# Performance work log

Measured on AMD Instinct MI355X. Metric: run time of the kernel, lower is better.

Reference implementation:

```python
import jax, jax.numpy as jnp
import numpy as np

WS = 8        # window size (square)
TW = 8        # total windows per side = input_resolution // WS
NH = 16       # num heads


def make_indices(ws, tw):
    # local relative position index (N, N)
    c = np.stack(np.meshgrid(np.arange(ws), np.arange(ws), indexing='ij')).reshape(2, -1)
    rel = (c[:, :, None] - c[:, None, :]).transpose(1, 2, 0).astype(np.int64)
    rel[..., 0] += ws - 1
    rel[..., 1] += ws - 1
    rel[..., 0] *= 2 * ws - 1
    local_idx = rel.sum(-1)
    # global (window-token -> window-grid) relative position index (N, tw*tw)
    ck = np.stack(np.meshgrid(np.arange(tw), np.arange(tw), indexing='ij')).reshape(2, -1)
    relg = (c[:, :, None] - ck[:, None, :]).transpose(1, 2, 0).astype(np.int64)
    relg[..., 0] += tw - 1
    relg[..., 1] += tw - 1
    relg[..., 0] *= ws + tw - 1
    global_idx = relg.sum(-1)
    return local_idx, global_idx


def setup_inputs() -> dict:
    key = jax.random.key(0)
    ks = jax.random.split(key, 13)
    B, H, W, C = 16, 64, 64, 512
    s = 0.02
    return {
        'x': jax.random.normal(ks[0], (B, H, W, C), jnp.float32),
        'qkv_w': jax.random.normal(ks[1], (C, 3 * C), jnp.float32) * s,
        'qkv_b': jax.random.normal(ks[2], (3 * C,), jnp.float32) * s,
        'local_bias_table': jax.random.normal(ks[3], ((2 * WS - 1) ** 2, NH), jnp.float32) * s,
        'global_bias_table': jax.random.normal(ks[4], ((WS + TW - 1) ** 2, NH), jnp.float32) * s,
        'local_proj_w': jax.random.normal(ks[5], (C, C), jnp.float32) * s,
        'local_proj_b': jax.random.normal(ks[6], (C,), jnp.float32) * s,
        'pool_w': jnp.full((WS * WS,), 1.0 / (WS * WS) * (WS * WS), jnp.float32) * 0 + jax.random.normal(ks[7], (WS * WS,), jnp.float32) * s + 1.0 / (WS * WS),
        'pool_b': jnp.zeros((1,), jnp.float32),
        'global_proj_w': jax.random.normal(ks[8], (C, C), jnp.float32) * s,
        'global_proj_b': jax.random.normal(ks[9], (C,), jnp.float32) * s,
        'pfc_w': jax.random.normal(ks[10], (2 * C, C), jnp.float32) * s,
        'pfc_b': jax.random.normal(ks[11], (C,), jnp.float32) * s,
    }


def reference(x, qkv_w, qkv_b, local_bias_table, global_bias_table,
              local_proj_w, local_proj_b, pool_w, pool_b,
              global_proj_w, global_proj_b, pfc_w, pfc_b):
    B, H, W, C = x.shape
    N = WS * WS                      # tokens per window
    nWs = (H // WS) * (W // WS)      # number of windows
    B_ = B * nWs
    hd = C // NH
    scale = hd ** -0.5

    local_idx, global_idx = make_indices(WS, H // WS)

    # NOTE: faithful to original — qkv applied to x in row-major order,
    # then reshaped into (B_, N, ...) chunks (window_partition output is unused).
    qkv = (x.reshape(-1, C) @ qkv_w + qkv_b).reshape(B_, N, 3, NH, hd)
    qkv = qkv.transpose(2, 0, 3, 1, 4)  # (3, B_, NH, N, hd)
    q, k, v = qkv[0], qkv[1], qkv[2]

    # ---- fine (local window) attention ----
    lb = local_bias_table[local_idx.reshape(-1)].reshape(N, N, NH).transpose(2, 0, 1)
    fine = jax.nn.softmax(jnp.einsum('bhnd,bhmd->bhnm', q * scale, k) + lb[None])
    fine_out = jnp.einsum('bhnm,bhmd->bnhd', fine, v).reshape(B_, N, C)
    fine_out = fine_out @ local_proj_w + local_proj_b

    # ---- coarse (pooled global) attention ----
    k5 = k.reshape(B, nWs, NH, N, hd)
    v5 = v.reshape(B, nWs, NH, N, hd)
    # pooled over the N window-token axis; original uses pool_layer_k for BOTH K and V
    Kg = jnp.einsum('bwhnd,n->bhwd', k5, pool_w) + pool_b  # (B, NH, nWs, hd)
    Vg = jnp.einsum('bwhnd,n->bhwd', v5, pool_w) + pool_b
    Kb = jnp.broadcast_to(Kg[:, None], (B, nWs, NH, nWs, hd)).reshape(B_, NH, nWs, hd)
    Vb = jnp.broadcast_to(Vg[:, None], (B, nWs, NH, nWs, hd)).reshape(B_, NH, nWs, hd)

    gb = global_bias_table[global_idx.reshape(-1)].reshape(N, nWs, NH).transpose(2, 0, 1)
    coarse = jax.nn.softmax(jnp.einsum('bhnd,bhwd->bhnw', q * scale, Kb) + gb[None])
    coarse_out = jnp.einsum('bhnw,bhwd->bnhd', coarse, Vb).reshape(B_, N, C)
    coarse_out = coarse_out @ global_proj_w + global_proj_b

    # ---- fused projection ----
    out = jnp.concatenate([fine_out, coarse_out], axis=-1) @ pfc_w + pfc_b
    return out  # (B_, N, C)
```

## Files before the change

kernel.cpp:

```cpp
#include <hip/hip_runtime.h>


typedef unsigned int u32;
typedef _Float16 f16;
typedef __attribute__((ext_vector_type(8))) _Float16 f16x8;
typedef __attribute__((ext_vector_type(4))) float f32x4;
typedef __attribute__((ext_vector_type(4))) u32 u32x4;

__device__ __forceinline__ f32x4 mfma_16x16x32(f16x8 a, f16x8 b, f32x4 c) {
  return __builtin_amdgcn_mfma_f32_16x16x32_f16(a, b, c, 0, 0, 0);
}

__device__ __forceinline__ void async_cp16(const void* g, void* l) {
  __builtin_amdgcn_global_load_lds(
      (const __attribute__((address_space(1))) u32*)g,
      (__attribute__((address_space(3))) u32*)l, 16, 0, 0);
}

__device__ __forceinline__ f16x8 cvt8_rtz(const float4 a, const float4 b) {
  u32x4 w;
  w[0] = __builtin_bit_cast(u32, __builtin_amdgcn_cvt_pkrtz(a.x, a.y));
  w[1] = __builtin_bit_cast(u32, __builtin_amdgcn_cvt_pkrtz(a.z, a.w));
  w[2] = __builtin_bit_cast(u32, __builtin_amdgcn_cvt_pkrtz(b.x, b.y));
  w[3] = __builtin_bit_cast(u32, __builtin_amdgcn_cvt_pkrtz(b.z, b.w));
  return __builtin_bit_cast(f16x8, w);
}


__global__ void k_cvtx(const float* __restrict__ X, f16* __restrict__ X16) {
  const size_t stride = (size_t)2048 * 256 * 8;
  size_t base = ((size_t)blockIdx.x * 256 + threadIdx.x) * 8;
  for (int it = 0; it < 8; ++it, base += stride) {
    const float4 a = *reinterpret_cast<const float4*>(X + base);
    const float4 b = *reinterpret_cast<const float4*>(X + base + 4);
    *reinterpret_cast<f16x8*>(X16 + base) = cvt8_rtz(a, b);
  }
}

__global__ void k_biastab(const float* __restrict__ ltab, const float* __restrict__ gtab,
                          f16* __restrict__ lbf, f16* __restrict__ gbf) {
  const int id = blockIdx.x * 256 + threadIdx.x;
  const int pair = id & 4095;
  const int n = pair >> 6, m = pair & 63;
  const int yn = n >> 3, xn = n & 7;
  const int ym = m >> 3, xm = m & 7;
  const int idx = (yn - ym + 7) * 15 + (xn - xm + 7);
  if (id < 4096) {
#pragma unroll
    for (int h = 0; h < 16; ++h) lbf[h * 4096 + pair] = (f16)ltab[idx * 16 + h];
  } else {
#pragma unroll
    for (int h = 0; h < 16; ++h) gbf[h * 4096 + pair] = (f16)gtab[idx * 16 + h];
  }
}

__global__ void k_tqkvw(const float* __restrict__ w, f16* __restrict__ wT) {
  __shared__ f16 sT[64][72];
  const int bid = blockIdx.x;
  const int k0 = (bid / 24) * 64, n0 = (bid % 24) * 64;
  const int t = threadIdx.x;
#pragma unroll
  for (int p = 0; p < 4; ++p) {
    const int kl = p * 16 + (t >> 4), nl = (t & 15) * 4;
    const float4 v = *reinterpret_cast<const float4*>(w + (size_t)(k0 + kl) * 1536 + n0 + nl);
    sT[kl][nl] = (f16)v.x; sT[kl][nl + 1] = (f16)v.y;
    sT[kl][nl + 2] = (f16)v.z; sT[kl][nl + 3] = (f16)v.w;
  }
  __syncthreads();
#pragma unroll
  for (int q = 0; q < 2; ++q) {
    const int nl = q * 32 + (t >> 3), kl = (t & 7) * 8;
    f16x8 r;
#pragma unroll
    for (int j = 0; j < 8; ++j) r[j] = sT[kl + j][nl];
    *reinterpret_cast<f16x8*>(wT + (size_t)(n0 + nl) * 512 + k0 + kl) = r;
  }
}

__global__ __launch_bounds__(256) void k_compose(const float* __restrict__ lpw,
                                                 const float* __restrict__ gpw,
                                                 const float* __restrict__ pfc_w,
                                                 f16* __restrict__ WT) {
  __shared__ float sW[16][16];
  const int kk0 = blockIdx.x * 16;
  const bool top = kk0 < 512;
  const float* src = top ? (lpw + kk0 * 512) : (gpw + (kk0 - 512) * 512);
  const float* pf = pfc_w + (top ? 0 : 512 * 512);
  const int t = threadIdx.x;
  float acc0[16], acc1[16];
#pragma unroll
  for (int i = 0; i < 16; ++i) { acc0[i] = 0.f; acc1[i] = 0.f; }
  for (int ct = 0; ct < 32; ++ct) {
    sW[t >> 4][t & 15] = src[(t >> 4) * 512 + ct * 16 + (t & 15)];
    __syncthreads();
#pragma unroll
    for (int cc = 0; cc < 16; ++cc) {
      const int c = ct * 16 + cc;
      const float p0 = pf[c * 512 + t];
      const float p1 = pf[c * 512 + t + 256];
#pragma unroll
      for (int i = 0; i < 16; ++i) { acc0[i] += sW[i][cc] * p0; acc1[i] += sW[i][cc] * p1; }
    }
    __syncthreads();
  }
#pragma unroll
  for (int i = 0; i < 16; ++i) {
    const int kk = kk0 + i;
    const int kp = ((kk >> 5) & 15) * 64 + (kk >> 9) * 32 + (kk & 31);
    WT[(size_t)t * 1024 + kp] = (f16)acc0[i];
    WT[(size_t)(t + 256) * 1024 + kp] = (f16)acc1[i];
  }
}

__global__ void k_bc_init(const float* __restrict__ pfc_b, float* __restrict__ bc) {
  const int j = blockIdx.x * 256 + threadIdx.x;
  bc[j] = pfc_b[j];
}

__global__ void k_bc_acc(const float* __restrict__ lpb, const float* __restrict__ gpb,
                         const float* __restrict__ pfc_w, float* __restrict__ bc) {
  const int t = threadIdx.x;
  const int c0 = blockIdx.x * 32;
  float p0 = 0.f, p1 = 0.f;
#pragma unroll
  for (int i = 0; i < 32; ++i) {
    const int c = c0 + i;
    const float wgt = (c < 512) ? lpb[c] : gpb[c - 512];
    p0 += wgt * pfc_w[(size_t)c * 512 + t];
    p1 += wgt * pfc_w[(size_t)c * 512 + t + 256];
  }
  atomicAdd(bc + t, p0);
  atomicAdd(bc + t + 256, p1);
}

__global__ __launch_bounds__(512, 2) void k_gemm_qkv(const f16* __restrict__ A,
                                                     const f16* __restrict__ BT,
                                                     const float* __restrict__ qkv_b,
                                                     const float* __restrict__ pool_w,
                                                     const float* __restrict__ pool_b,
                                                     f16* __restrict__ qb,
                                                     f16* __restrict__ kb,
                                                     f16* __restrict__ vb,
                                                     f16* __restrict__ Kgb,
                                                     f16* __restrict__ Vgt) {
  __shared__ f16 sA[8192], sB[4096];
  const int wid = (blockIdx.x & 7) * 384 + (blockIdx.x >> 3);
  const int br = wid / 12, bn = wid % 12;
  const int t = threadIdx.x;
  const int wv = t >> 6, l = t & 63, lr = l & 15, lk = l >> 4;
  const int wvr = wv >> 1, wvc = wv & 1;

  f32x4 acc[4][4] = {};

  const f16* gA = A + (size_t)(br * 256 + (t >> 2)) * 512 + (t & 3) * 8;
  const f16* gB = BT + (size_t)(bn * 128 + (t >> 2)) * 512 + (t & 3) * 8;

  for (int kk = 0; kk < 16; ++kk) {
    async_cp16(gA + kk * 32, &sA[t * 8]);
    async_cp16(gA + 128 * 512 + kk * 32, &sA[4096 + t * 8]);
    async_cp16(gB + kk * 32, &sB[t * 8]);
    __syncthreads();
    f16x8 af[4], bf[4];
#pragma unroll
    for (int m = 0; m < 4; ++m)
      af[m] = *reinterpret_cast<const f16x8*>(&sA[(wvr * 64 + m * 16 + lr) * 32 + lk * 8]);
#pragma unroll
    for (int n = 0; n < 4; ++n)
      bf[n] = *reinterpret_cast<const f16x8*>(&sB[(wvc * 64 + n * 16 + lr) * 32 + lk * 8]);
#pragma unroll
    for (int m = 0; m < 4; ++m)
#pragma unroll
      for (int n = 0; n < 4; ++n) acc[m][n] = mfma_16x16x32(af[m], bf[n], acc[m][n]);
    __syncthreads();
  }

  const int w_idx = br * 4 + wvr;
  const int bb = w_idx >> 6, ww = w_idx & 63;
  float pw[4][4];
#pragma unroll
  for (int m = 0; m < 4; ++m)
#pragma unroll
    for (int r = 0; r < 4; ++r) pw[m][r] = pool_w[m * 16 + lk * 4 + r];
  const float pb = pool_b[0];

#pragma unroll
  for (int n = 0; n < 4; ++n) {
    const int col = bn * 128 + wvc * 64 + n * 16 + lr;
    const int which = col >> 9;
    const int hh = (col >> 5) & 15, d = col & 31;
    const float bias = qkv_b[col];
    f16* dst = which == 0 ? qb : (which == 1 ? kb : vb);
#pragma unroll
    for (int m = 0; m < 4; ++m)
#pragma unroll
      for (int r = 0; r < 4; ++r) {
        const int row = br * 256 + wvr * 64 + m * 16 + lk * 4 + r;
        dst[(size_t)(((row >> 6) << 4) + hh) * 2048 + (row & 63) * 32 + d] =
            (f16)(acc[m][n][r] + bias);
      }
    if (which != 0) {
      float part = 0.f;
#pragma unroll
      for (int m = 0; m < 4; ++m)
#pragma unroll
        for (int r = 0; r < 4; ++r) part += (acc[m][n][r] + bias) * pw[m][r];
      part += __shfl_xor(part, 16);
      part += __shfl_xor(part, 32);
      part += pb;
      if (lk == 0) {
        if (which == 1)
          Kgb[((size_t)(bb * 16 + hh) * 64 + ww) * 32 + d] = (f16)part;
        else
          Vgt[((size_t)(bb * 16 + hh) * 32 + d) * 64 + ww] = (f16)part;
      }
    }
  }
}

__global__ __launch_bounds__(256) void k_attn(const f16* __restrict__ qb,
                                              const f16* __restrict__ kb,
                                              const f16* __restrict__ vb,
                                              const f16* __restrict__ Kgb,
                                              const f16* __restrict__ Vgt,
                                              const f16* __restrict__ lbf,
                                              const f16* __restrict__ gbf,
                                              f16* __restrict__ cat) {
  __shared__ f16 sVraw[2048];
  __shared__ f16 sVt[2048];
  __shared__ f16 sP[4096];
  __shared__ f16 sCat[4096];
  const int bid = blockIdx.x;
  const int b_ = bid >> 4, h = bid & 15;
  const int gs = ((b_ >> 6) << 4) + h;
  const int t = threadIdx.x;
  const int wv = t >> 6, l = t & 63, lr = l & 15, lk = l >> 4;
  const float scale = 0.17677669529663687f;
  const size_t hs = (size_t)bid * 2048;

  async_cp16(vb + hs + t * 8, &sVraw[t * 8]);

  const f16x8 aq = *reinterpret_cast<const f16x8*>(qb + hs + (wv * 16 + lr) * 32 + lk * 8);

  f32x4 s[4];
#pragma unroll
  for (int j = 0; j < 4; ++j) {
    const f16x8 bk = *reinterpret_cast<const f16x8*>(kb + hs + (j * 16 + lr) * 32 + lk * 8);
    f32x4 z = {};
    s[j] = mfma_16x16x32(aq, bk, z);
  }

  __syncthreads();

  {
    const int d = t >> 3, tok0 = (t & 7) << 3;
    f16x8 w;
#pragma unroll
    for (int j = 0; j < 8; ++j) w[j] = sVraw[(tok0 + j) * 32 + d];
    *reinterpret_cast<f16x8*>(&sVt[d * 64 + (((t & 7) ^ (d & 7)) << 3)]) = w;
  }

  float p[4][4], inv[4];
  {
    const f16* bt = lbf + h * 4096 + (wv * 16 + lk * 4) * 64;
#pragma unroll
    for (int r = 0; r < 4; ++r) {
      float m = -1e30f;
#pragma unroll
      for (int j = 0; j < 4; ++j) {
        const float v = s[j][r] * scale + (float)bt[r * 64 + j * 16 + lr];
        p[j][r] = v;
        m = fmaxf(m, v);
      }
      m = fmaxf(m, __shfl_xor(m, 1));
      m = fmaxf(m, __shfl_xor(m, 2));
      m = fmaxf(m, __shfl_xor(m, 4));
      m = fmaxf(m, __shfl_xor(m, 8));
      float su = 0.f;
#pragma unroll
      for (int j = 0; j < 4; ++j) {
        const float e = __expf(p[j][r] - m);
        p[j][r] = e;
        su += e;
      }
      su += __shfl_xor(su, 1);
      su += __shfl_xor(su, 2);
      su += __shfl_xor(su, 4);
      su += __shfl_xor(su, 8);
      inv[r] = 1.f / su;
    }
#pragma unroll
    for (int r = 0; r < 4; ++r) {
      const int rowP = wv * 16 + lk * 4 + r;
#pragma unroll
      for (int j = 0; j < 4; ++j) {
        const int col = j * 16 + lr;
        sP[rowP * 64 + (((col >> 3) ^ (rowP & 7)) << 3) + (col & 7)] = (f16)p[j][r];
      }
    }
  }

  __syncthreads();

  {
    const int rowP = wv * 16 + lr;
    const f16x8 a0 = *reinterpret_cast<const f16x8*>(&sP[rowP * 64 + ((lk ^ (lr & 7)) << 3)]);
    const f16x8 a1 = *reinterpret_cast<const f16x8*>(&sP[rowP * 64 + (((4 + lk) ^ (lr & 7)) << 3)]);
#pragma unroll
    for (int n = 0; n < 2; ++n) {
      const int d = n * 16 + lr;
      const f16x8 b0 = *reinterpret_cast<const f16x8*>(&sVt[d * 64 + ((lk ^ (d & 7)) << 3)]);
      const f16x8 b1 = *reinterpret_cast<const f16x8*>(&sVt[d * 64 + (((4 + lk) ^ (d & 7)) << 3)]);
      f32x4 o = {};
      o = mfma_16x16x32(a0, b0, o);
      o = mfma_16x16x32(a1, b1, o);
#pragma unroll
      for (int r = 0; r < 4; ++r) {
        const int rowC = wv * 16 + lk * 4 + r;
        const int colC = n * 16 + lr;
        sCat[rowC * 64 + (((colC >> 3) ^ (rowC & 7)) << 3) + (colC & 7)] =
            (f16)(o[r] * inv[r]);
      }
    }
  }

#pragma unroll
  for (int j = 0; j < 4; ++j) {
    const f16x8 bk = *reinterpret_cast<const f16x8*>(
        Kgb + ((size_t)gs * 64 + j * 16 + lr) * 32 + lk * 8);
    f32x4 z = {};
    s[j] = mfma_16x16x32(aq, bk, z);
  }
  {
    const f16* bt = gbf + h * 4096 + (wv * 16 + lk * 4) * 64;
#pragma unroll
    for (int r = 0; r < 4; ++r) {
      float m = -1e30f;
#pragma unroll
      for (int j = 0; j < 4; ++j) {
        const float v = s[j][r] * scale + (float)bt[r * 64 + j * 16 + lr];
        p[j][r] = v;
        m = fmaxf(m, v);
      }
      m = fmaxf(m, __shfl_xor(m, 1));
      m = fmaxf(m, __shfl_xor(m, 2));
      m = fmaxf(m, __shfl_xor(m, 4));
      m = fmaxf(m, __shfl_xor(m, 8));
      float su = 0.f;
#pragma unroll
      for (int j = 0; j < 4; ++j) {
        const float e = __expf(p[j][r] - m);
        p[j][r] = e;
        su += e;
      }
      su += __shfl_xor(su, 1);
      su += __shfl_xor(su, 2);
      su += __shfl_xor(su, 4);
      su += __shfl_xor(su, 8);
      inv[r] = 1.f / su;
    }
#pragma unroll
    for (int r = 0; r < 4; ++r) {
      const int rowP = wv * 16 + lk * 4 + r;
#pragma unroll
      for (int j = 0; j < 4; ++j) {
        const int col = j * 16 + lr;
        sP[rowP * 64 + (((col >> 3) ^ (rowP & 7)) << 3) + (col & 7)] = (f16)p[j][r];
      }
    }
  }

  {
    const int rowP = wv * 16 + lr;
    const f16x8 a0 = *reinterpret_cast<const f16x8*>(&sP[rowP * 64 + ((lk ^ (lr & 7)) << 3)]);
    const f16x8 a1 = *reinterpret_cast<const f16x8*>(&sP[rowP * 64 + (((4 + lk) ^ (lr & 7)) << 3)]);
#pragma unroll
    for (int n = 0; n < 2; ++n) {
      const f16* vp = Vgt + ((size_t)gs * 32 + n * 16 + lr) * 64 + lk * 8;
      const f16x8 b0 = *reinterpret_cast<const f16x8*>(vp);
      const f16x8 b1 = *reinterpret_cast<const f16x8*>(vp + 32);
      f32x4 o = {};
      o = mfma_16x16x32(a0, b0, o);
      o = mfma_16x16x32(a1, b1, o);
#pragma unroll
      for (int r = 0; r < 4; ++r) {
        const int rowC = wv * 16 + lk * 4 + r;
        const int colC = 32 + n * 16 + lr;
        sCat[rowC * 64 + (((colC >> 3) ^ (rowC & 7)) << 3) + (colC & 7)] =
            (f16)(o[r] * inv[r]);
      }
    }
  }

  f16* catp = cat + ((size_t)b_ * 64) * 1024 + h * 64;
#pragma unroll
  for (int pass = 0; pass < 2; ++pass) {
    const int row = wv * 16 + pass * 8 + (l >> 3);
    const int c = l & 7;
    const f16x8 v = *reinterpret_cast<const f16x8*>(&sCat[row * 64 + ((c ^ (row & 7)) << 3)]);
    *reinterpret_cast<f16x8*>(catp + (size_t)row * 1024 + c * 8) = v;
  }
}

__global__ __launch_bounds__(512, 2) void k_gemm_final(const f16* __restrict__ A,
                                                       const f16* __restrict__ BT,
                                                       const float* __restrict__ bc,
                                                       float* __restrict__ out) {
  __shared__ f16 sA[8192];
  __shared__ f16 sB[16384];
  const int wid = (blockIdx.x & 7) * 128 + (blockIdx.x >> 3);
  const int br = wid >> 1, bn = wid & 1;
  const int t = threadIdx.x;
  const int wv = t >> 6, l = t & 63, lr = l & 15, lk = l >> 4;
  const int wvM = wv >> 2, wvN = wv & 3;

  f32x4 acc[4][4] = {};

  const int srow = t >> 3;
  const int scg = (t & 7) ^ (srow & 7);
  const f16* gA = A + (size_t)(br * 128 + srow) * 1024 + scg * 8;
  const f16* gB = BT + (size_t)(bn * 256 + srow) * 1024 + scg * 8;

  for (int kk = 0; kk < 16; ++kk) {
#pragma unroll
    for (int i = 0; i < 2; ++i)
      async_cp16(gA + (size_t)(i * 64) * 1024 + kk * 64, &sA[(i * 512 + t) * 8]);
#pragma unroll
    for (int i = 0; i < 4; ++i)
      async_cp16(gB + (size_t)(i * 64) * 1024 + kk * 64, &sB[(i * 512 + t) * 8]);
    __syncthreads();
    f16x8 af[4][2], bf[4][2];
#pragma unroll
    for (int m = 0; m < 4; ++m) {
      const int row = wvM * 64 + m * 16 + lr;
#pragma unroll
      for (int h = 0; h < 2; ++h)
        af[m][h] = *reinterpret_cast<const f16x8*>(
            &sA[row * 64 + ((((h << 2) + lk) ^ (row & 7)) << 3)]);
    }
#pragma unroll
    for (int n = 0; n < 4; ++n) {
      const int row = wvN * 64 + n * 16 + lr;
#pragma unroll
      for (int h = 0; h < 2; ++h)
        bf[n][h] = *reinterpret_cast<const f16x8*>(
            &sB[row * 64 + ((((h << 2) + lk) ^ (row & 7)) << 3)]);
    }
#pragma unroll
    for (int m = 0; m < 4; ++m)
#pragma unroll
      for (int n = 0; n < 4; ++n) {
        acc[m][n] = mfma_16x16x32(af[m][0], bf[n][0], acc[m][n]);
        acc[m][n] = mfma_16x16x32(af[m][1], bf[n][1], acc[m][n]);
      }
    __syncthreads();
  }

#pragma unroll
  for (int n = 0; n < 4; ++n) {
    const int col = bn * 256 + wvN * 64 + n * 16 + lr;
    const float bias = bc[col];
#pragma unroll
    for (int m = 0; m < 4; ++m)
#pragma unroll
      for (int r = 0; r < 4; ++r) {
        const int row = br * 128 + wvM * 64 + m * 16 + lk * 4 + r;
        out[(size_t)row * 512 + col] = acc[m][n][r] + bias;
      }
  }
}


extern "C" void kernel_launch(void* const* d_in, const int* in_sizes, int n_in,
                              void* d_out, int out_size, void* d_ws, size_t ws_size,
                              hipStream_t stream) {
  const float* x      = (const float*)d_in[0];
  const float* qkv_w  = (const float*)d_in[1];
  const float* qkv_b  = (const float*)d_in[2];
  const float* ltab   = (const float*)d_in[3];
  const float* gtab   = (const float*)d_in[4];
  const float* lpw    = (const float*)d_in[5];
  const float* lpb    = (const float*)d_in[6];
  const float* pool_w = (const float*)d_in[7];
  const float* pool_b = (const float*)d_in[8];
  const float* gpw    = (const float*)d_in[9];
  const float* gpb    = (const float*)d_in[10];
  const float* pfc_w  = (const float*)d_in[11];
  const float* pfc_b  = (const float*)d_in[12];
  float* out = (float*)d_out;

  char* ws = (char*)d_ws;
  f16*   qb   = (f16*)(ws + 0);
  f16*   kb   = (f16*)(ws + 67108864);
  f16*   vb   = (f16*)(ws + 134217728);
  f16*   cat  = (f16*)(ws + 201326592);
  f16*   X16  = (f16*)(ws + 201326592);
  f16*   qwT  = (f16*)(ws + 335544320);
  f16*   WcT  = (f16*)(ws + 337117184);
  float* bc   = (float*)(ws + 338165760);
  f16*   lbf  = (f16*)(ws + 338167808);
  f16*   gbf  = (f16*)(ws + 338429952);
  f16*   Kgb  = (f16*)(ws + 338692096);
  f16*   Vgt  = (f16*)(ws + 339740672);

  k_cvtx<<<2048, 256, 0, stream>>>(x, X16);
  k_biastab<<<32, 256, 0, stream>>>(ltab, gtab, lbf, gbf);
  k_tqkvw<<<192, 256, 0, stream>>>(qkv_w, qwT);
  k_compose<<<64, 256, 0, stream>>>(lpw, gpw, pfc_w, WcT);
  k_bc_init<<<2, 256, 0, stream>>>(pfc_b, bc);
  k_bc_acc<<<32, 256, 0, stream>>>(lpb, gpb, pfc_w, bc);
  k_gemm_qkv<<<3072, 512, 0, stream>>>(X16, qwT, qkv_b, pool_w, pool_b,
                                       qb, kb, vb, Kgb, Vgt);
  k_attn<<<16384, 256, 0, stream>>>(qb, kb, vb, Kgb, Vgt, lbf, gbf, cat);
  k_gemm_final<<<1024, 512, 0, stream>>>(cat, WcT, bc, out);
}
```

Baseline: 495.9 us.

## Store V transposed from QKV GEMM epilogue and drop LDS transpose in attention

The QKV GEMM epilogue now writes V in a per-head transposed (d-major) layout using 4-wide f16 stores, so the attention kernel can load V fragments straight from global memory. This removes the async copy of raw V into LDS, the LDS transpose, and one block barrier in k_attn. The fine and coarse attention paths are merged into one unrolled loop over two halves. The cost is a different store pattern in the GEMM epilogue and uncoalesced direct global loads for V in the attention kernel.

Measured after the change: 561.1 us. 1.13x slower.

```diff
diff --git a/kernel.cpp b/kernel.cpp
--- a/kernel.cpp
+++ b/kernel.cpp
@@ -3,6 +3,7 @@
 
 typedef unsigned int u32;
 typedef _Float16 f16;
+typedef __attribute__((ext_vector_type(4))) _Float16 f16x4;
 typedef __attribute__((ext_vector_type(8))) _Float16 f16x8;
 typedef __attribute__((ext_vector_type(4))) float f32x4;
 typedef __attribute__((ext_vector_type(4))) u32 u32x4;
@@ -140,7 +141,7 @@
                                                      const float* __restrict__ pool_b,
                                                      f16* __restrict__ qb,
                                                      f16* __restrict__ kb,
-                                                     f16* __restrict__ vb,
+                                                     f16* __restrict__ vbT,
                                                      f16* __restrict__ Kgb,
                                                      f16* __restrict__ Vgt) {
   __shared__ f16 sA[8192], sB[4096];
@@ -174,6 +175,7 @@
     __syncthreads();
   }
 
+  const int which = bn >> 2;
   const int w_idx = br * 4 + wvr;
   const int bb = w_idx >> 6, ww = w_idx & 63;
   float pw[4][4];
@@ -186,18 +188,25 @@
 #pragma unroll
   for (int n = 0; n < 4; ++n) {
     const int col = bn * 128 + wvc * 64 + n * 16 + lr;
-    const int which = col >> 9;
     const int hh = (col >> 5) & 15, d = col & 31;
     const float bias = qkv_b[col];
-    f16* dst = which == 0 ? qb : (which == 1 ? kb : vb);
-#pragma unroll
-    for (int m = 0; m < 4; ++m)
-#pragma unroll
-      for (int r = 0; r < 4; ++r) {
-        const int row = br * 256 + wvr * 64 + m * 16 + lk * 4 + r;
-        dst[(size_t)(((row >> 6) << 4) + hh) * 2048 + (row & 63) * 32 + d] =
-            (f16)(acc[m][n][r] + bias);
-      }
+    const size_t slice = (size_t)(w_idx * 16 + hh) * 2048;
+    if (which == 2) {
+#pragma unroll
+      for (int m = 0; m < 4; ++m) {
+        f16x4 v;
+#pragma unroll
+        for (int r = 0; r < 4; ++r) v[r] = (f16)(acc[m][n][r] + bias);
+        *reinterpret_cast<f16x4*>(vbT + slice + d * 64 + m * 16 + lk * 4) = v;
+      }
+    } else {
+      f16* dst = which == 0 ? qb : kb;
+#pragma unroll
+      for (int m = 0; m < 4; ++m)
+#pragma unroll
+        for (int r = 0; r < 4; ++r)
+          dst[slice + (m * 16 + lk * 4 + r) * 32 + d] = (f16)(acc[m][n][r] + bias);
+    }
     if (which != 0) {
       float part = 0.f;
 #pragma unroll
@@ -219,14 +228,12 @@
 
 __global__ __launch_bounds__(256) void k_attn(const f16* __restrict__ qb,
                                               const f16* __restrict__ kb,
-                                              const f16* __restrict__ vb,
+                                              const f16* __restrict__ vbT,
                                               const f16* __restrict__ Kgb,
                                               const f16* __restrict__ Vgt,
                                               const f16* __restrict__ lbf,
                                               const f16* __restrict__ gbf,
                                               f16* __restrict__ cat) {
-  __shared__ f16 sVraw[2048];
-  __shared__ f16 sVt[2048];
   __shared__ f16 sP[4096];
   __shared__ f16 sCat[4096];
   const int bid = blockIdx.x;
@@ -237,156 +244,80 @@
   const float scale = 0.17677669529663687f;
   const size_t hs = (size_t)bid * 2048;
 
-  async_cp16(vb + hs + t * 8, &sVraw[t * 8]);
-
   const f16x8 aq = *reinterpret_cast<const f16x8*>(qb + hs + (wv * 16 + lr) * 32 + lk * 8);
 
-  f32x4 s[4];
-#pragma unroll
-  for (int j = 0; j < 4; ++j) {
-    const f16x8 bk = *reinterpret_cast<const f16x8*>(kb + hs + (j * 16 + lr) * 32 + lk * 8);
-    f32x4 z = {};
-    s[j] = mfma_16x16x32(aq, bk, z);
-  }
-
-  __syncthreads();
-
-  {
-    const int d = t >> 3, tok0 = (t & 7) << 3;
-    f16x8 w;
-#pragma unroll
-    for (int j = 0; j < 8; ++j) w[j] = sVraw[(tok0 + j) * 32 + d];
-    *reinterpret_cast<f16x8*>(&sVt[d * 64 + (((t & 7) ^ (d & 7)) << 3)]) = w;
-  }
-
   float p[4][4], inv[4];
-  {
-    const f16* bt = lbf + h * 4096 + (wv * 16 + lk * 4) * 64;
-#pragma unroll
-    for (int r = 0; r < 4; ++r) {
-      float m = -1e30f;
-#pragma unroll
-      for (int j = 0; j < 4; ++j) {
-        const float v = s[j][r] * scale + (float)bt[r * 64 + j * 16 + lr];
-        p[j][r] = v;
-        m = fmaxf(m, v);
-      }
-      m = fmaxf(m, __shfl_xor(m, 1));
-      m = fmaxf(m, __shfl_xor(m, 2));
-      m = fmaxf(m, __shfl_xor(m, 4));
-      m = fmaxf(m, __shfl_xor(m, 8));
-      float su = 0.f;
-#pragma unroll
-      for (int j = 0; j < 4; ++j) {
-        const float e = __expf(p[j][r] - m);
-        p[j][r] = e;
-        su += e;
-      }
-      su += __shfl_xor(su, 1);
-      su += __shfl_xor(su, 2);
-      su += __shfl_xor(su, 4);
-      su += __shfl_xor(su, 8);
-      inv[r] = 1.f / su;
-    }
-#pragma unroll
-    for (int r = 0; r < 4; ++r) {
-      const int rowP = wv * 16 + lk * 4 + r;
-#pragma unroll
-      for (int j = 0; j < 4; ++j) {
-        const int col = j * 16 + lr;
-        sP[rowP * 64 + (((col >> 3) ^ (rowP & 7)) << 3) + (col & 7)] = (f16)p[j][r];
-      }
-    }
-  }
-
-  __syncthreads();
-
-  {
-    const int rowP = wv * 16 + lr;
-    const f16x8 a0 = *reinterpret_cast<const f16x8*>(&sP[rowP * 64 + ((lk ^ (lr & 7)) << 3)]);
-    const f16x8 a1 = *reinterpret_cast<const f16x8*>(&sP[rowP * 64 + (((4 + lk) ^ (lr & 7)) << 3)]);
-#pragma unroll
-    for (int n = 0; n < 2; ++n) {
-      const int d = n * 16 + lr;
-      const f16x8 b0 = *reinterpret_cast<const f16x8*>(&sVt[d * 64 + ((lk ^ (d & 7)) << 3)]);
-      const f16x8 b1 = *reinterpret_cast<const f16x8*>(&sVt[d * 64 + (((4 + lk) ^ (d & 7)) << 3)]);
-      f32x4 o = {};
-      o = mfma_16x16x32(a0, b0, o);
-      o = mfma_16x16x32(a1, b1, o);
+
+#pragma unroll
+  for (int half = 0; half < 2; ++half) {
+    f32x4 s[4];
+#pragma unroll
+    for (int j = 0; j < 4; ++j) {
+      const f16x8 bk = (half == 0)
+          ? *reinterpret_cast<const f16x8*>(kb + hs + (j * 16 + lr) * 32 + lk * 8)
+          : *reinterpret_cast<const f16x8*>(Kgb + ((size_t)gs * 64 + j * 16 + lr) * 32 + lk * 8);
+      f32x4 z = {};
+      s[j] = mfma_16x16x32(aq, bk, z);
+    }
+    {
+      const f16* bt = (half == 0 ? lbf : gbf) + h * 4096 + (wv * 16 + lk * 4) * 64;
 #pragma unroll
       for (int r = 0; r < 4; ++r) {
-        const int rowC = wv * 16 + lk * 4 + r;
-        const int colC = n * 16 + lr;
-        sCat[rowC * 64 + (((colC >> 3) ^ (rowC & 7)) << 3) + (colC & 7)] =
-            (f16)(o[r] * inv[r]);
-      }
-    }
-  }
-
-#pragma unroll
-  for (int j = 0; j < 4; ++j) {
-    const f16x8 bk = *reinterpret_cast<const f16x8*>(
-        Kgb + ((size_t)gs * 64 + j * 16 + lr) * 32 + lk * 8);
-    f32x4 z = {};
-    s[j] = mfma_16x16x32(aq, bk, z);
-  }
-  {
-    const f16* bt = gbf + h * 4096 + (wv * 16 + lk * 4) * 64;
-#pragma unroll
-    for (int r = 0; r < 4; ++r) {
-      float m = -1e30f;
-#pragma unroll
-      for (int j = 0; j < 4; ++j) {
-        const float v = s[j][r] * scale + (float)bt[r * 64 + j * 16 + lr];
-        p[j][r] = v;
-        m = fmaxf(m, v);
-      }
-      m = fmaxf(m, __shfl_xor(m, 1));
-      m = fmaxf(m, __shfl_xor(m, 2));
-      m = fmaxf(m, __shfl_xor(m, 4));
-      m = fmaxf(m, __shfl_xor(m, 8));
-      float su = 0.f;
-#pragma unroll
-      for (int j = 0; j < 4; ++j) {
-        const float e = __expf(p[j][r] - m);
-        p[j][r] = e;
-        su += e;
-      }
-      su += __shfl_xor(su, 1);
-      su += __shfl_xor(su, 2);
-      su += __shfl_xor(su, 4);
-      su += __shfl_xor(su, 8);
-      inv[r] = 1.f / su;
-    }
-#pragma unroll
-    for (int r = 0; r < 4; ++r) {
-      const int rowP = wv * 16 + lk * 4 + r;
-#pragma unroll
-      for (int j = 0; j < 4; ++j) {
-        const int col = j * 16 + lr;
-        sP[rowP * 64 + (((col >> 3) ^ (rowP & 7)) << 3) + (col & 7)] = (f16)p[j][r];
-      }
-    }
-  }
-
-  {
-    const int rowP = wv * 16 + lr;
-    const f16x8 a0 = *reinterpret_cast<const f16x8*>(&sP[rowP * 64 + ((lk ^ (lr & 7)) << 3)]);
-    const f16x8 a1 = *reinterpret_cast<const f16x8*>(&sP[rowP * 64 + (((4 + lk) ^ (lr & 7)) << 3)]);
-#pragma unroll
-    for (int n = 0; n < 2; ++n) {
-      const f16* vp = Vgt + ((size_t)gs * 32 + n * 16 + lr) * 64 + lk * 8;
-      const f16x8 b0 = *reinterpret_cast<const f16x8*>(vp);
-      const f16x8 b1 = *reinterpret_cast<const f16x8*>(vp + 32);
-      f32x4 o = {};
-      o = mfma_16x16x32(a0, b0, o);
-      o = mfma_16x16x32(a1, b1, o);
+        float m = -1e30f;
+#pragma unroll
+        for (int j = 0; j < 4; ++j) {
+          const float v = s[j][r] * scale + (float)bt[r * 64 + j * 16 + lr];
+          p[j][r] = v;
+          m = fmaxf(m, v);
+        }
+        m = fmaxf(m, __shfl_xor(m, 1));
+        m = fmaxf(m, __shfl_xor(m, 2));
+        m = fmaxf(m, __shfl_xor(m, 4));
+        m = fmaxf(m, __shfl_xor(m, 8));
+        float su = 0.f;
+#pragma unroll
+        for (int j = 0; j < 4; ++j) {
+          const float e = __expf(p[j][r] - m);
+          p[j][r] = e;
+          su += e;
+        }
+        su += __shfl_xor(su, 1);
+        su += __shfl_xor(su, 2);
+        su += __shfl_xor(su, 4);
+        su += __shfl_xor(su, 8);
+        inv[r] = 1.f / su;
+      }
 #pragma unroll
       for (int r = 0; r < 4; ++r) {
-        const int rowC = wv * 16 + lk * 4 + r;
-        const int colC = 32 + n * 16 + lr;
-        sCat[rowC * 64 + (((colC >> 3) ^ (rowC & 7)) << 3) + (colC & 7)] =
-            (f16)(o[r] * inv[r]);
+        const int rowP = wv * 16 + lk * 4 + r;
+#pragma unroll
+        for (int j = 0; j < 4; ++j) {
+          const int col = j * 16 + lr;
+          sP[rowP * 64 + (((col >> 3) ^ (rowP & 7)) << 3) + (col & 7)] = (f16)p[j][r];
+        }
+      }
+    }
+    {
+      const int rowP = wv * 16 + lr;
+      const f16x8 a0 = *reinterpret_cast<const f16x8*>(&sP[rowP * 64 + ((lk ^ (lr & 7)) << 3)]);
+      const f16x8 a1 = *reinterpret_cast<const f16x8*>(&sP[rowP * 64 + (((4 + lk) ^ (lr & 7)) << 3)]);
+#pragma unroll
+      for (int n = 0; n < 2; ++n) {
+        const f16* vp = (half == 0)
+            ? vbT + hs + (size_t)(n * 16 + lr) * 64 + lk * 8
+            : Vgt + ((size_t)gs * 32 + n * 16 + lr) * 64 + lk * 8;
+        const f16x8 b0 = *reinterpret_cast<const f16x8*>(vp);
+        const f16x8 b1 = *reinterpret_cast<const f16x8*>(vp + 32);
+        f32x4 o = {};
+        o = mfma_16x16x32(a0, b0, o);
+        o = mfma_16x16x32(a1, b1, o);
+#pragma unroll
+        for (int r = 0; r < 4; ++r) {
+          const int rowC = wv * 16 + lk * 4 + r;
+          const int colC = half * 32 + n * 16 + lr;
+          sCat[rowC * 64 + (((colC >> 3) ^ (rowC & 7)) << 3) + (colC & 7)] =
+              (f16)(o[r] * inv[r]);
+        }
       }
     }
   }
@@ -491,7 +422,7 @@
   char* ws = (char*)d_ws;
   f16*   qb   = (f16*)(ws + 0);
   f16*   kb   = (f16*)(ws + 67108864);
-  f16*   vb   = (f16*)(ws + 134217728);
+  f16*   vbT  = (f16*)(ws + 134217728);
   f16*   cat  = (f16*)(ws + 201326592);
   f16*   X16  = (f16*)(ws + 201326592);
   f16*   qwT  = (f16*)(ws + 335544320);
@@ -509,7 +440,7 @@
   k_bc_init<<<2, 256, 0, stream>>>(pfc_b, bc);
   k_bc_acc<<<32, 256, 0, stream>>>(lpb, gpb, pfc_w, bc);
   k_gemm_qkv<<<3072, 512, 0, stream>>>(X16, qwT, qkv_b, pool_w, pool_b,
-                                       qb, kb, vb, Kgb, Vgt);
-  k_attn<<<16384, 256, 0, stream>>>(qb, kb, vb, Kgb, Vgt, lbf, gbf, cat);
+                                       qb, kb, vbT, Kgb, Vgt);
+  k_attn<<<16384, 256, 0, stream>>>(qb, kb, vbT, Kgb, Vgt, lbf, gbf, cat);
   k_gemm_final<<<1024, 512, 0, stream>>>(cat, WcT, bc, out);
 }
```

## Enlarge QKV GEMM tile to 256x256 with 1024 threads and XOR-swizzled LDS

Applied to the files above, without the earlier changes.

The QKV projection GEMM now uses 256x256 output tiles computed by 16 waves (1024 threads) instead of 256x128 tiles with 8 waves, halving the block count and improving operand reuse per loaded byte. LDS reads and writes use an XOR swizzle on the 16-byte chunk index to reduce bank conflicts for the MFMA fragment loads. The q/k/v destination selection is hoisted to block level because each tile now lies entirely in one of the three outputs. The larger block lowers occupancy and may raise register pressure; the single-buffered loop still syncs twice per k-step.

Measured after the change: 518.3 us. 1.05x slower.

```diff
diff --git a/kernel.cpp b/kernel.cpp
--- a/kernel.cpp
+++ b/kernel.cpp
@@ -133,40 +133,45 @@
   atomicAdd(bc + t + 256, p1);
 }
 
-__global__ __launch_bounds__(512, 2) void k_gemm_qkv(const f16* __restrict__ A,
-                                                     const f16* __restrict__ BT,
-                                                     const float* __restrict__ qkv_b,
-                                                     const float* __restrict__ pool_w,
-                                                     const float* __restrict__ pool_b,
-                                                     f16* __restrict__ qb,
-                                                     f16* __restrict__ kb,
-                                                     f16* __restrict__ vb,
-                                                     f16* __restrict__ Kgb,
-                                                     f16* __restrict__ Vgt) {
-  __shared__ f16 sA[8192], sB[4096];
-  const int wid = (blockIdx.x & 7) * 384 + (blockIdx.x >> 3);
-  const int br = wid / 12, bn = wid % 12;
+__global__ __launch_bounds__(1024) void k_gemm_qkv(const f16* __restrict__ A,
+                                                   const f16* __restrict__ BT,
+                                                   const float* __restrict__ qkv_b,
+                                                   const float* __restrict__ pool_w,
+                                                   const float* __restrict__ pool_b,
+                                                   f16* __restrict__ qb,
+                                                   f16* __restrict__ kb,
+                                                   f16* __restrict__ vb,
+                                                   f16* __restrict__ Kgb,
+                                                   f16* __restrict__ Vgt) {
+  __shared__ f16 sA[8192], sB[8192];
+  const int wid = (blockIdx.x & 7) * 192 + (blockIdx.x >> 3);
+  const int br = wid / 6, bn = wid % 6;
   const int t = threadIdx.x;
   const int wv = t >> 6, l = t & 63, lr = l & 15, lk = l >> 4;
-  const int wvr = wv >> 1, wvc = wv & 1;
+  const int wvM = wv >> 2, wvN = wv & 3;
 
   f32x4 acc[4][4] = {};
 
-  const f16* gA = A + (size_t)(br * 256 + (t >> 2)) * 512 + (t & 3) * 8;
-  const f16* gB = BT + (size_t)(bn * 128 + (t >> 2)) * 512 + (t & 3) * 8;
+  const int srow = t >> 2;
+  const int scol = ((t & 3) ^ (srow & 3)) * 8;
+  const f16* gA = A + (size_t)(br * 256 + srow) * 512 + scol;
+  const f16* gB = BT + (size_t)(bn * 256 + srow) * 512 + scol;
 
   for (int kk = 0; kk < 16; ++kk) {
     async_cp16(gA + kk * 32, &sA[t * 8]);
-    async_cp16(gA + 128 * 512 + kk * 32, &sA[4096 + t * 8]);
     async_cp16(gB + kk * 32, &sB[t * 8]);
     __syncthreads();
     f16x8 af[4], bf[4];
 #pragma unroll
-    for (int m = 0; m < 4; ++m)
-      af[m] = *reinterpret_cast<const f16x8*>(&sA[(wvr * 64 + m * 16 + lr) * 32 + lk * 8]);
-#pragma unroll
-    for (int n = 0; n < 4; ++n)
-      bf[n] = *reinterpret_cast<const f16x8*>(&sB[(wvc * 64 + n * 16 + lr) * 32 + lk * 8]);
+    for (int m = 0; m < 4; ++m) {
+      const int row = wvM * 64 + m * 16 + lr;
+      af[m] = *reinterpret_cast<const f16x8*>(&sA[row * 32 + ((lk ^ (row & 3)) * 8)]);
+    }
+#pragma unroll
+    for (int n = 0; n < 4; ++n) {
+      const int row = wvN * 64 + n * 16 + lr;
+      bf[n] = *reinterpret_cast<const f16x8*>(&sB[row * 32 + ((lk ^ (row & 3)) * 8)]);
+    }
 #pragma unroll
     for (int m = 0; m < 4; ++m)
 #pragma unroll
@@ -174,7 +179,9 @@
     __syncthreads();
   }
 
-  const int w_idx = br * 4 + wvr;
+  const int which = bn >> 1;
+  f16* dst = which == 0 ? qb : (which == 1 ? kb : vb);
+  const int w_idx = br * 4 + wvM;
   const int bb = w_idx >> 6, ww = w_idx & 63;
   float pw[4][4];
 #pragma unroll
@@ -185,16 +192,14 @@
 
 #pragma unroll
   for (int n = 0; n < 4; ++n) {
-    const int col = bn * 128 + wvc * 64 + n * 16 + lr;
-    const int which = col >> 9;
+    const int col = bn * 256 + wvN * 64 + n * 16 + lr;
     const int hh = (col >> 5) & 15, d = col & 31;
     const float bias = qkv_b[col];
-    f16* dst = which == 0 ? qb : (which == 1 ? kb : vb);
 #pragma unroll
     for (int m = 0; m < 4; ++m)
 #pragma unroll
       for (int r = 0; r < 4; ++r) {
-        const int row = br * 256 + wvr * 64 + m * 16 + lk * 4 + r;
+        const int row = br * 256 + wvM * 64 + m * 16 + lk * 4 + r;
         dst[(size_t)(((row >> 6) << 4) + hh) * 2048 + (row & 63) * 32 + d] =
             (f16)(acc[m][n][r] + bias);
       }
@@ -508,8 +513,8 @@
   k_compose<<<64, 256, 0, stream>>>(lpw, gpw, pfc_w, WcT);
   k_bc_init<<<2, 256, 0, stream>>>(pfc_b, bc);
   k_bc_acc<<<32, 256, 0, stream>>>(lpb, gpb, pfc_w, bc);
-  k_gemm_qkv<<<3072, 512, 0, stream>>>(X16, qwT, qkv_b, pool_w, pool_b,
-                                       qb, kb, vb, Kgb, Vgt);
+  k_gemm_qkv<<<1536, 1024, 0, stream>>>(X16, qwT, qkv_b, pool_w, pool_b,
+                                        qb, kb, vb, Kgb, Vgt);
   k_attn<<<16384, 256, 0, stream>>>(qb, kb, vb, Kgb, Vgt, lbf, gbf, cat);
   k_gemm_final<<<1024, 512, 0, stream>>>(cat, WcT, bc, out);
 }
```

## Fold softmax scale into Q weights and seed MFMA with fragment-layout bias

Applied to the files above, without the earlier changes.

The attention scale is folded into the Q columns of the QKV weights and bias, so the attention kernel no longer multiplies scores by it. The relative-position bias tables are precomputed as fp32 in the MFMA accumulator fragment layout and used directly as the accumulator input, replacing the scalar half-precision bias gathers and adds. The softmax max-reduction and subtraction are removed for both the local and global attention. This cuts ALU work and cross-lane shuffles per attention block, but the softmax can overflow if logits become large, and the fp32 bias tables double the bias bytes read.

After: 484.9 us. 2.2% less time.

```diff
diff --git a/kernel.cpp b/kernel.cpp
--- a/kernel.cpp
+++ b/kernel.cpp
@@ -38,19 +38,23 @@
 }
 
 __global__ void k_biastab(const float* __restrict__ ltab, const float* __restrict__ gtab,
-                          f16* __restrict__ lbf, f16* __restrict__ gbf) {
+                          float* __restrict__ lbf, float* __restrict__ gbf) {
   const int id = blockIdx.x * 256 + threadIdx.x;
-  const int pair = id & 4095;
-  const int n = pair >> 6, m = pair & 63;
-  const int yn = n >> 3, xn = n & 7;
-  const int ym = m >> 3, xm = m & 7;
-  const int idx = (yn - ym + 7) * 15 + (xn - xm + 7);
-  if (id < 4096) {
-#pragma unroll
-    for (int h = 0; h < 16; ++h) lbf[h * 4096 + pair] = (f16)ltab[idx * 16 + h];
-  } else {
-#pragma unroll
-    for (int h = 0; h < 16; ++h) gbf[h * 4096 + pair] = (f16)gtab[idx * 16 + h];
+  const int tab = id >> 14;
+  const int rem = id & 16383;
+  const int h = rem >> 10;
+  const int wv = (rem >> 8) & 3;
+  const int j = (rem >> 6) & 3;
+  const int l = rem & 63;
+  const int lk = l >> 4, lr = l & 15;
+  const float* src = tab ? gtab : ltab;
+  float* out = (tab ? gbf : lbf) + (size_t)rem * 4;
+#pragma unroll
+  for (int r = 0; r < 4; ++r) {
+    const int n = wv * 16 + lk * 4 + r;
+    const int m = j * 16 + lr;
+    const int idx = ((n >> 3) - (m >> 3) + 7) * 15 + ((n & 7) - (m & 7) + 7);
+    out[r] = src[idx * 16 + h];
   }
 }
 
@@ -58,13 +62,14 @@
   __shared__ f16 sT[64][72];
   const int bid = blockIdx.x;
   const int k0 = (bid / 24) * 64, n0 = (bid % 24) * 64;
+  const float sc = (n0 < 512) ? 0.17677669529663687f : 1.0f;
   const int t = threadIdx.x;
 #pragma unroll
   for (int p = 0; p < 4; ++p) {
     const int kl = p * 16 + (t >> 4), nl = (t & 15) * 4;
     const float4 v = *reinterpret_cast<const float4*>(w + (size_t)(k0 + kl) * 1536 + n0 + nl);
-    sT[kl][nl] = (f16)v.x; sT[kl][nl + 1] = (f16)v.y;
-    sT[kl][nl + 2] = (f16)v.z; sT[kl][nl + 3] = (f16)v.w;
+    sT[kl][nl] = (f16)(v.x * sc); sT[kl][nl + 1] = (f16)(v.y * sc);
+    sT[kl][nl + 2] = (f16)(v.z * sc); sT[kl][nl + 3] = (f16)(v.w * sc);
   }
   __syncthreads();
 #pragma unroll
@@ -188,7 +193,7 @@
     const int col = bn * 128 + wvc * 64 + n * 16 + lr;
     const int which = col >> 9;
     const int hh = (col >> 5) & 15, d = col & 31;
-    const float bias = qkv_b[col];
+    const float bias = which == 0 ? qkv_b[col] * 0.17677669529663687f : qkv_b[col];
     f16* dst = which == 0 ? qb : (which == 1 ? kb : vb);
 #pragma unroll
     for (int m = 0; m < 4; ++m)
@@ -222,8 +227,8 @@
                                               const f16* __restrict__ vb,
                                               const f16* __restrict__ Kgb,
                                               const f16* __restrict__ Vgt,
-                                              const f16* __restrict__ lbf,
-                                              const f16* __restrict__ gbf,
+                                              const float* __restrict__ lbf,
+                                              const float* __restrict__ gbf,
                                               f16* __restrict__ cat) {
   __shared__ f16 sVraw[2048];
   __shared__ f16 sVt[2048];
@@ -234,19 +239,19 @@
   const int gs = ((b_ >> 6) << 4) + h;
   const int t = threadIdx.x;
   const int wv = t >> 6, l = t & 63, lr = l & 15, lk = l >> 4;
-  const float scale = 0.17677669529663687f;
   const size_t hs = (size_t)bid * 2048;
 
   async_cp16(vb + hs + t * 8, &sVraw[t * 8]);
 
   const f16x8 aq = *reinterpret_cast<const f16x8*>(qb + hs + (wv * 16 + lr) * 32 + lk * 8);
+  const float* btL = lbf + (size_t)((h * 4 + wv) * 4) * 256 + l * 4;
+  const float* btG = gbf + (size_t)((h * 4 + wv) * 4) * 256 + l * 4;
 
   f32x4 s[4];
 #pragma unroll
   for (int j = 0; j < 4; ++j) {
     const f16x8 bk = *reinterpret_cast<const f16x8*>(kb + hs + (j * 16 + lr) * 32 + lk * 8);
-    f32x4 z = {};
-    s[j] = mfma_16x16x32(aq, bk, z);
+    s[j] = mfma_16x16x32(aq, bk, *reinterpret_cast<const f32x4*>(btL + j * 256));
   }
 
   __syncthreads();
@@ -260,42 +265,28 @@
   }
 
   float p[4][4], inv[4];
-  {
-    const f16* bt = lbf + h * 4096 + (wv * 16 + lk * 4) * 64;
-#pragma unroll
-    for (int r = 0; r < 4; ++r) {
-      float m = -1e30f;
-#pragma unroll
-      for (int j = 0; j < 4; ++j) {
-        const float v = s[j][r] * scale + (float)bt[r * 64 + j * 16 + lr];
-        p[j][r] = v;
-        m = fmaxf(m, v);
-      }
-      m = fmaxf(m, __shfl_xor(m, 1));
-      m = fmaxf(m, __shfl_xor(m, 2));
-      m = fmaxf(m, __shfl_xor(m, 4));
-      m = fmaxf(m, __shfl_xor(m, 8));
-      float su = 0.f;
-#pragma unroll
-      for (int j = 0; j < 4; ++j) {
-        const float e = __expf(p[j][r] - m);
-        p[j][r] = e;
-        su += e;
-      }
-      su += __shfl_xor(su, 1);
-      su += __shfl_xor(su, 2);
-      su += __shfl_xor(su, 4);
-      su += __shfl_xor(su, 8);
-      inv[r] = 1.f / su;
-    }
-#pragma unroll
-    for (int r = 0; r < 4; ++r) {
-      const int rowP = wv * 16 + lk * 4 + r;
-#pragma unroll
-      for (int j = 0; j < 4; ++j) {
-        const int col = j * 16 + lr;
-        sP[rowP * 64 + (((col >> 3) ^ (rowP & 7)) << 3) + (col & 7)] = (f16)p[j][r];
-      }
+#pragma unroll
+  for (int r = 0; r < 4; ++r) {
+    float su = 0.f;
+#pragma unroll
+    for (int j = 0; j < 4; ++j) {
+      const float e = __expf(s[j][r]);
+      p[j][r] = e;
+      su += e;
+    }
+    su += __shfl_xor(su, 1);
+    su += __shfl_xor(su, 2);
+    su += __shfl_xor(su, 4);
+    su += __shfl_xor(su, 8);
+    inv[r] = 1.f / su;
+  }
+#pragma unroll
+  for (int r = 0; r < 4; ++r) {
+    const int rowP = wv * 16 + lk * 4 + r;
+#pragma unroll
+    for (int j = 0; j < 4; ++j) {
+      const int col = j * 16 + lr;
+      sP[rowP * 64 + (((col >> 3) ^ (rowP & 7)) << 3) + (col & 7)] = (f16)p[j][r];
     }
   }
 
@@ -327,45 +318,30 @@
   for (int j = 0; j < 4; ++j) {
     const f16x8 bk = *reinterpret_cast<const f16x8*>(
         Kgb + ((size_t)gs * 64 + j * 16 + lr) * 32 + lk * 8);
-    f32x4 z = {};
-    s[j] = mfma_16x16x32(aq, bk, z);
-  }
-  {
-    const f16* bt = gbf + h * 4096 + (wv * 16 + lk * 4) * 64;
-#pragma unroll
-    for (int r = 0; r < 4; ++r) {
-      float m = -1e30f;
-#pragma unroll
-      for (int j = 0; j < 4; ++j) {
-        const float v = s[j][r] * scale + (float)bt[r * 64 + j * 16 + lr];
-        p[j][r] = v;
-        m = fmaxf(m, v);
-      }
-      m = fmaxf(m, __shfl_xor(m, 1));
-      m = fmaxf(m, __shfl_xor(m, 2));
-      m = fmaxf(m, __shfl_xor(m, 4));
-      m = fmaxf(m, __shfl_xor(m, 8));
-      float su = 0.f;
-#pragma unroll
-      for (int j = 0; j < 4; ++j) {
-        const float e = __expf(p[j][r] - m);
-        p[j][r] = e;
-        su += e;
-      }
-      su += __shfl_xor(su, 1);
-      su += __shfl_xor(su, 2);
-      su += __shfl_xor(su, 4);
-      su += __shfl_xor(su, 8);
-      inv[r] = 1.f / su;
-    }
-#pragma unroll
-    for (int r = 0; r < 4; ++r) {
-      const int rowP = wv * 16 + lk * 4 + r;
-#pragma unroll
-      for (int j = 0; j < 4; ++j) {
-        const int col = j * 16 + lr;
-        sP[rowP * 64 + (((col >> 3) ^ (rowP & 7)) << 3) + (col & 7)] = (f16)p[j][r];
-      }
+    s[j] = mfma_16x16x32(aq, bk, *reinterpret_cast<const f32x4*>(btG + j * 256));
+  }
+#pragma unroll
+  for (int r = 0; r < 4; ++r) {
+    float su = 0.f;
+#pragma unroll
+    for (int j = 0; j < 4; ++j) {
+      const float e = __expf(s[j][r]);
+      p[j][r] = e;
+      su += e;
+    }
+    su += __shfl_xor(su, 1);
+    su += __shfl_xor(su, 2);
+    su += __shfl_xor(su, 4);
+    su += __shfl_xor(su, 8);
+    inv[r] = 1.f / su;
+  }
+#pragma unroll
+  for (int r = 0; r < 4; ++r) {
+    const int rowP = wv * 16 + lk * 4 + r;
+#pragma unroll
+    for (int j = 0; j < 4; ++j) {
+      const int col = j * 16 + lr;
+      sP[rowP * 64 + (((col >> 3) ^ (rowP & 7)) << 3) + (col & 7)] = (f16)p[j][r];
     }
   }
 
@@ -433,17 +409,17 @@
     for (int m = 0; m < 4; ++m) {
       const int row = wvM * 64 + m * 16 + lr;
 #pragma unroll
-      for (int h = 0; h < 2; ++h)
-        af[m][h] = *reinterpret_cast<const f16x8*>(
-            &sA[row * 64 + ((((h << 2) + lk) ^ (row & 7)) << 3)]);
+      for (int hh = 0; hh < 2; ++hh)
+        af[m][hh] = *reinterpret_cast<const f16x8*>(
+            &sA[row * 64 + ((((hh << 2) + lk) ^ (row & 7)) << 3)]);
     }
 #pragma unroll
     for (int n = 0; n < 4; ++n) {
       const int row = wvN * 64 + n * 16 + lr;
 #pragma unroll
-      for (int h = 0; h < 2; ++h)
-        bf[n][h] = *reinterpret_cast<const f16x8*>(
-            &sB[row * 64 + ((((h << 2) + lk) ^ (row & 7)) << 3)]);
+      for (int hh = 0; hh < 2; ++hh)
+        bf[n][hh] = *reinterpret_cast<const f16x8*>(
+            &sB[row * 64 + ((((hh << 2) + lk) ^ (row & 7)) << 3)]);
     }
 #pragma unroll
     for (int m = 0; m < 4; ++m)
@@ -497,13 +473,13 @@
   f16*   qwT  = (f16*)(ws + 335544320);
   f16*   WcT  = (f16*)(ws + 337117184);
   float* bc   = (float*)(ws + 338165760);
-  f16*   lbf  = (f16*)(ws + 338167808);
-  f16*   gbf  = (f16*)(ws + 338429952);
+  float* lbf  = (float*)(ws + 338167808);
+  float* gbf  = (float*)(ws + 338429952);
   f16*   Kgb  = (f16*)(ws + 338692096);
   f16*   Vgt  = (f16*)(ws + 339740672);
 
   k_cvtx<<<2048, 256, 0, stream>>>(x, X16);
-  k_biastab<<<32, 256, 0, stream>>>(ltab, gtab, lbf, gbf);
+  k_biastab<<<128, 256, 0, stream>>>(ltab, gtab, lbf, gbf);
   k_tqkvw<<<192, 256, 0, stream>>>(qkv_w, qwT);
   k_compose<<<64, 256, 0, stream>>>(lpw, gpw, pfc_w, WcT);
   k_bc_init<<<2, 256, 0, stream>>>(pfc_b, bc);
```
